# Optimization experiments

Measured on AMD Instinct MI355X. Metric: run time of the kernel, lower is better.

## Reference

```python
import jax, jax.numpy as jnp
import numpy as np

N_NODES = 50000
N_EDGES = 800000
IN_DIM = 256
OUT_DIM = 32
HEADS = 4
NEG_SLOPE = 0.2  # PyG GATConv default
LN_EPS = 1e-5


def setup_inputs() -> dict:
    key = jax.random.key(0)
    ks = jax.random.split(key, 8)
    x = jax.random.normal(ks[0], (N_NODES, IN_DIM), dtype=jnp.float32)
    edge_index = jax.random.randint(ks[1], (2, N_EDGES), 0, N_NODES, dtype=jnp.int64)
    # Glorot-ish scaling for stability
    W = jax.random.normal(ks[2], (IN_DIM, HEADS * OUT_DIM), dtype=jnp.float32) / np.sqrt(IN_DIM)
    att_src = jax.random.normal(ks[3], (HEADS, OUT_DIM), dtype=jnp.float32) / np.sqrt(OUT_DIM)
    att_dst = jax.random.normal(ks[4], (HEADS, OUT_DIM), dtype=jnp.float32) / np.sqrt(OUT_DIM)
    bias = jax.random.normal(ks[5], (HEADS * OUT_DIM,), dtype=jnp.float32) * 0.02
    gamma = jnp.ones((HEADS * OUT_DIM,), dtype=jnp.float32)
    beta = jnp.zeros((HEADS * OUT_DIM,), dtype=jnp.float32)
    return {"x": x, "edge_index": edge_index, "W": W, "att_src": att_src,
            "att_dst": att_dst, "bias": bias, "gamma": gamma, "beta": beta}


def reference(x, edge_index, W, att_src, att_dst, bias, gamma, beta):
    N = x.shape[0]
    H, C = att_src.shape
    # --- GATConv (PyG semantics, eval mode so attention dropout is identity) ---
    # add self-loops (PyG default add_self_loops=True)
    loops = jnp.arange(N, dtype=edge_index.dtype)
    src = jnp.concatenate([edge_index[0], loops])  # [E+N]
    dst = jnp.concatenate([edge_index[1], loops])
    h = (x @ W).reshape(N, H, C)                    # [N,H,C] (lin has no bias)
    a_s = jnp.einsum('nhc,hc->nh', h, att_src)      # [N,H]
    a_d = jnp.einsum('nhc,hc->nh', h, att_dst)
    e = jax.nn.leaky_relu(a_s[src] + a_d[dst], NEG_SLOPE)  # [E+N,H]
    # segment softmax over incoming edges of each destination node
    emax = jax.ops.segment_max(e, dst, num_segments=N)     # every node has a self-loop
    ee = jnp.exp(e - emax[dst])
    denom = jax.ops.segment_sum(ee, dst, num_segments=N)
    alpha = ee / denom[dst]                                 # [E+N,H]
    msg = h[src] * alpha[:, :, None]                        # [E+N,H,C]
    out = jax.ops.segment_sum(msg, dst, num_segments=N).reshape(N, H * C) + bias
    # --- LayerNorm ---
    mu = out.mean(-1, keepdims=True)
    var = ((out - mu) ** 2).mean(-1, keepdims=True)
    out = (out - mu) * jax.lax.rsqrt(var + LN_EPS) * gamma + beta
    # --- dropout (eval: identity) + ELU ---
    return jax.nn.elu(out)
```

## Files before the change

### kernel.cpp

```cpp
#include <hip/hip_runtime.h>
#include <hip/hip_bf16.h>
#include <cstdint>
#include <cstddef>

#define N_NODES 50000
#define N_EDGES 800000
#define IN_DIM 256
#define HC 128
#define HEADS 4
#define NEG_SLOPE 0.2f
#define LN_EPS 1e-5f

#define NGB ((N_NODES + 63) / 64)
#define CAP 64
#define NBUCK 196
#define CAP_PB 32

typedef _Float16 f16x8 __attribute__((ext_vector_type(8)));
typedef _Float16 f16x2 __attribute__((ext_vector_type(2)));
typedef float f32x4 __attribute__((ext_vector_type(4)));

__device__ __forceinline__ float lrelu(float x) { return x > 0.f ? x : NEG_SLOPE * x; }
__device__ __forceinline__ unsigned pack_h2(float a, float b) {
    f16x2 h; h[0] = (_Float16)a; h[1] = (_Float16)b;
    return *(unsigned*)&h;
}

__global__ __launch_bounds__(256) void k_prep_passA(
    const float* __restrict__ W, const int* __restrict__ ei,
    _Float16* __restrict__ W16,
    int* __restrict__ cnt_tab, int2* __restrict__ arena)
{
    __shared__ int cnt[256];
    const int tid = threadIdx.x;
    const int b = blockIdx.x;

    if (b < 16) {
        int c = b * 256 + tid;
        int col = c & 15, quad = (c >> 4) & 3, nt = (c >> 6) & 7, kt = c >> 9;
        int n = nt * 16 + col;
        f16x8 v;
#pragma unroll
        for (int j = 0; j < 8; ++j) {
            int k = kt * 32 + quad * 8 + j;
            v[j] = (_Float16)W[k * HC + n];
        }
        *(f16x8*)(W16 + (size_t)c * 8) = v;
        return;
    }

    const int blk = b - 16;
    const int eb = blk << 10;
    cnt[tid] = 0;
    __syncthreads();
    int src[4], dst[4], rk[4], bk[4];
    bool valid[4];
#pragma unroll
    for (int it = 0; it < 4; ++it) {
        int e = eb + it * 256 + tid;
        valid[it] = (e < N_EDGES);
        src[it] = 0; dst[it] = 0; bk[it] = 0; rk[it] = 0;
        if (valid[it]) {
            src[it] = ei[e];
            dst[it] = ei[N_EDGES + e];
            bk[it]  = dst[it] >> 8;
            rk[it]  = atomicAdd(&cnt[bk[it]], 1);
        }
    }
#pragma unroll
    for (int it = 0; it < 4; ++it) {
        if (valid[it]) {
            int p = ((bk[it] * NGB + blk) << 5) + rk[it];
            arena[p] = (int2){src[it], dst[it]};
        }
    }
    __syncthreads();
    if (tid < NBUCK) cnt_tab[blk * NBUCK + tid] = cnt[tid];
}

__global__ __launch_bounds__(256) void k_gemm(
    const float* __restrict__ x, const _Float16* __restrict__ W16,
    const float* __restrict__ att_src, const float* __restrict__ att_dst,
    _Float16* __restrict__ h16, float* __restrict__ a_s, float* __restrict__ a_d)
{
    __shared__ _Float16 Wlds[32768];
    const int tid = threadIdx.x;

    const int wave = tid >> 6;
    const int lane = tid & 63;
    const int col  = lane & 15;
    const int quad = lane >> 4;
    const int m0   = blockIdx.x * 64 + wave * 16;

    const int rowA = min(m0 + col, N_NODES - 1);
    const float* xrow = x + (size_t)rowA * IN_DIM + quad * 8;

    float4 xr[16];
#pragma unroll
    for (int kt = 0; kt < 8; ++kt) {
        xr[2 * kt]     = *(const float4*)(xrow + kt * 32);
        xr[2 * kt + 1] = *(const float4*)(xrow + kt * 32 + 4);
    }

    {
        const uint4* g4 = (const uint4*)W16;
        uint4* s4 = (uint4*)Wlds;
#pragma unroll
        for (int it = 0; it < 16; ++it) s4[it * 256 + tid] = g4[it * 256 + tid];
    }
    __syncthreads();

    f32x4 acc[8];
#pragma unroll
    for (int nt = 0; nt < 8; ++nt) acc[nt] = (f32x4){0.f, 0.f, 0.f, 0.f};

#pragma unroll
    for (int kt = 0; kt < 8; ++kt) {
        float4 xa = xr[2 * kt], xb = xr[2 * kt + 1];
        f16x8 a;
        a[0] = (_Float16)xa.x; a[1] = (_Float16)xa.y;
        a[2] = (_Float16)xa.z; a[3] = (_Float16)xa.w;
        a[4] = (_Float16)xb.x; a[5] = (_Float16)xb.y;
        a[6] = (_Float16)xb.z; a[7] = (_Float16)xb.w;
#pragma unroll
        for (int nt = 0; nt < 8; ++nt) {
            f16x8 bb = *(const f16x8*)&Wlds[((kt * 8 + nt) * 64 + quad * 16 + col) * 8];
            acc[nt] = __builtin_amdgcn_mfma_f32_16x16x32_f16(a, bb, acc[nt], 0, 0, 0);
        }
    }

    f16x2* h2g = (f16x2*)h16;
#pragma unroll
    for (int a2 = 0; a2 < 4; ++a2) {
#pragma unroll
        for (int r = 0; r < 4; ++r) {
            int row = m0 + quad * 4 + r;
            if (row < N_NODES) {
                f16x2 hv;
                hv[0] = (_Float16)acc[2 * a2][r];
                hv[1] = (_Float16)acc[2 * a2 + 1][r];
                h2g[(size_t)row * 64 + a2 * 16 + col] = hv;
            }
        }
    }

    float pS[4][4], pD[4][4];
#pragma unroll
    for (int hd = 0; hd < 4; ++hd)
#pragma unroll
        for (int r = 0; r < 4; ++r) { pS[hd][r] = 0.f; pD[hd][r] = 0.f; }

#pragma unroll
    for (int nt = 0; nt < 8; ++nt) {
        int ch = nt * 16 + col;
        float sv = att_src[ch], dv = att_dst[ch];
        int hd = nt >> 1;
#pragma unroll
        for (int r = 0; r < 4; ++r) {
            pS[hd][r] += acc[nt][r] * sv;
            pD[hd][r] += acc[nt][r] * dv;
        }
    }
#pragma unroll
    for (int off = 1; off < 16; off <<= 1) {
#pragma unroll
        for (int hd = 0; hd < 4; ++hd)
#pragma unroll
            for (int r = 0; r < 4; ++r) {
                pS[hd][r] += __shfl_xor(pS[hd][r], off, 16);
                pD[hd][r] += __shfl_xor(pD[hd][r], off, 16);
            }
    }
    if (col == 0) {
#pragma unroll
        for (int r = 0; r < 4; ++r) {
            int row = m0 + quad * 4 + r;
            if (row < N_NODES) {
#pragma unroll
                for (int hd = 0; hd < 4; ++hd) {
                    a_s[row * HEADS + hd] = pS[hd][r];
                    a_d[row * HEADS + hd] = pD[hd][r];
                }
            }
        }
    }
}

__global__ __launch_bounds__(1024) void k_bucket(
    const int2* __restrict__ arena, const int* __restrict__ cnt_tab,
    int* __restrict__ rec, int* __restrict__ counts)
{
    __shared__ int cnt[256];
    const int b = blockIdx.x, tid = threadIdx.x;
    if (tid < 256) cnt[tid] = 0;
    __syncthreads();
    if (tid < NGB) {
        int m = cnt_tab[tid * NBUCK + b];
        const int2* seg = arena + (((size_t)b * NGB + tid) << 5);
        for (int i = 0; i < m; ++i) {
            int2 ed = seg[i];
            int r = atomicAdd(&cnt[ed.y & 255], 1);
            rec[((size_t)ed.y << 6) + r] = ed.x;
        }
    }
    __syncthreads();
    if (tid < 256) {
        int n = (b << 8) + tid;
        if (n < N_NODES) counts[n] = cnt[tid];
    }
}

__global__ __launch_bounds__(256) void k_gather(
    const int* __restrict__ counts, const int* __restrict__ rec,
    const float* __restrict__ a_s, const float* __restrict__ a_d,
    const _Float16* __restrict__ h16, const float* __restrict__ bias,
    const float* __restrict__ gamma, const float* __restrict__ beta,
    float* __restrict__ out)
{
    __shared__ int   lsrc[256];
    __shared__ uint2 lw[256];

    int gid = blockIdx.x * 256 + threadIdx.x;
    int n = gid >> 6, lane = gid & 63;
    if (n >= N_NODES) return;

    const int wbase = (threadIdx.x >> 6) * 64;
    const int beg = n << 6;
    const int deg = counts[n];
    const int hd = lane >> 4;
    const f16x2* h2 = (const f16x2*)h16;
    const unsigned short* lwh = (const unsigned short*)&lw[wbase];

    const float4 ad4 = *(const float4*)(a_d + (size_t)n * HEADS);
    const float adh = (hd == 0) ? ad4.x : (hd == 1) ? ad4.y : (hd == 2) ? ad4.z : ad4.w;
    const float wSelf = __expf(lrelu(a_s[n * HEADS + hd] + adh));
    float den = wSelf;
    f16x2 hv = h2[(size_t)n * 64 + lane];
    float acc0 = (float)hv[0] * wSelf;
    float acc1 = (float)hv[1] * wSelf;

    for (int base = 0; base < deg; base += 64) {
        int nc = min(64, deg - base);
        if (lane < nc) {
            int src = rec[beg + base + lane];
            lsrc[wbase + lane] = src;
            float4 s4 = *(const float4*)(a_s + (size_t)src * HEADS);
            float w0 = __expf(lrelu(s4.x + ad4.x));
            float w1 = __expf(lrelu(s4.y + ad4.y));
            float w2 = __expf(lrelu(s4.z + ad4.z));
            float w3 = __expf(lrelu(s4.w + ad4.w));
            lw[wbase + lane] = (uint2){pack_h2(w0, w1), pack_h2(w2, w3)};
        }
        int j = 0;
        for (; j + 8 <= nc; j += 8) {
            int s[8]; float w[8]; f16x2 hh[8];
#pragma unroll
            for (int k = 0; k < 8; ++k) {
                s[k] = lsrc[wbase + j + k];
                unsigned short uw = lwh[(j + k) * 4 + hd];
                _Float16 wf = *(_Float16*)&uw;
                w[k] = (float)wf;
            }
#pragma unroll
            for (int k = 0; k < 8; ++k) hh[k] = h2[(size_t)s[k] * 64 + lane];
#pragma unroll
            for (int k = 0; k < 8; ++k) {
                acc0 += (float)hh[k][0] * w[k];
                acc1 += (float)hh[k][1] * w[k];
                den  += w[k];
            }
        }
        for (; j < nc; ++j) {
            int s0 = lsrc[wbase + j];
            unsigned short uw = lwh[j * 4 + hd];
            _Float16 wf = *(_Float16*)&uw;
            float w0 = (float)wf;
            f16x2 hx = h2[(size_t)s0 * 64 + lane];
            acc0 += (float)hx[0] * w0;
            acc1 += (float)hx[1] * w0;
            den  += w0;
        }
    }

    const int c0 = (lane >> 4) * 32 + (lane & 15);
    const int c1 = c0 + 16;
    float v0 = acc0 / den + bias[c0];
    float v1 = acc1 / den + bias[c1];
    float s = v0 + v1;
#pragma unroll
    for (int off = 32; off; off >>= 1) s += __shfl_xor(s, off, 64);
    float mu = s * (1.f / 128.f);
    float d0 = v0 - mu, d1 = v1 - mu;
    float q = d0 * d0 + d1 * d1;
#pragma unroll
    for (int off = 32; off; off >>= 1) q += __shfl_xor(q, off, 64);
    float rs = rsqrtf(q * (1.f / 128.f) + LN_EPS);
    float o0 = d0 * rs * gamma[c0] + beta[c0];
    float o1 = d1 * rs * gamma[c1] + beta[c1];
    o0 = o0 > 0.f ? o0 : __expf(o0) - 1.f;
    o1 = o1 > 0.f ? o1 : __expf(o1) - 1.f;
    out[(size_t)n * HC + c0] = o0;
    out[(size_t)n * HC + c1] = o1;
}

extern "C" void kernel_launch(void* const* d_in, const int* in_sizes, int n_in,
                              void* d_out, int out_size, void* d_ws, size_t ws_size,
                              hipStream_t stream) {
    const float* x       = (const float*)d_in[0];
    const int*   ei      = (const int*)d_in[1];
    const float* W       = (const float*)d_in[2];
    const float* att_src = (const float*)d_in[3];
    const float* att_dst = (const float*)d_in[4];
    const float* bias    = (const float*)d_in[5];
    const float* gamma   = (const float*)d_in[6];
    const float* beta    = (const float*)d_in[7];
    float* out = (float*)d_out;

    char* ws = (char*)d_ws;
    _Float16* h16     = (_Float16*)(ws);
    float*    a_s     = (float*)(ws + 12800000);
    float*    a_d     = (float*)(ws + 13600000);
    int*      rec     = (int*)  (ws + 14400000);
    int*      counts  = (int*)  (ws + 27200000);
    int*      cnt_tab = (int*)  (ws + 27400000);
    int2*     arena   = (int2*) (ws + 28020000);
    _Float16* W16     = (_Float16*)(ws + 67260000);

    k_prep_passA<<<16 + NGB, 256, 0, stream>>>(W, ei, W16, cnt_tab, arena);
    k_gemm<<<NGB, 256, 0, stream>>>(x, W16, att_src, att_dst, h16, a_s, a_d);
    k_bucket<<<NBUCK, 1024, 0, stream>>>(arena, cnt_tab, rec, counts);
    k_gather<<<(N_NODES * 64 + 255) / 256, 256, 0, stream>>>(
        counts, rec, a_s, a_d, h16, bias, gamma, beta, out);
}
```

Baseline: 177.2 us.

## Fuse GEMM and bucket scatter into one interleaved kernel launch

Merges the projection GEMM and the edge bucketing pass into one kernel. Odd blocks do bucketing and even blocks do a 256-row GEMM tile with 1024 threads. This removes a launch and lets the memory-bound scatter overlap the compute-bound GEMM on the same device. In exchange, GEMM blocks get larger (256 rows each), which cuts GEMM parallelism to about 196 blocks, and each block needs heavier LDS and register use.

```diff
diff --git a/kernel.cpp b/kernel.cpp
--- a/kernel.cpp
+++ b/kernel.cpp
@@ -11,7 +11,8 @@
 #define NEG_SLOPE 0.2f
 #define LN_EPS 1e-5f
 
-#define NGB ((N_NODES + 63) / 64)
+#define NGB ((N_NODES + 255) / 256)
+#define NPB 782
 #define CAP 64
 #define NBUCK 196
 #define CAP_PB 32
@@ -70,7 +71,7 @@
 #pragma unroll
     for (int it = 0; it < 4; ++it) {
         if (valid[it]) {
-            int p = ((bk[it] * NGB + blk) << 5) + rk[it];
+            int p = ((bk[it] * NPB + blk) << 5) + rk[it];
             arena[p] = (int2){src[it], dst[it]};
         }
     }
@@ -78,19 +79,45 @@
     if (tid < NBUCK) cnt_tab[blk * NBUCK + tid] = cnt[tid];
 }
 
-__global__ __launch_bounds__(256) void k_gemm(
+__global__ __launch_bounds__(1024) void k_gemm_bucket(
     const float* __restrict__ x, const _Float16* __restrict__ W16,
     const float* __restrict__ att_src, const float* __restrict__ att_dst,
-    _Float16* __restrict__ h16, float* __restrict__ a_s, float* __restrict__ a_d)
+    _Float16* __restrict__ h16, float* __restrict__ a_s, float* __restrict__ a_d,
+    const int2* __restrict__ arena, const int* __restrict__ cnt_tab,
+    int* __restrict__ rec, int* __restrict__ counts)
 {
     __shared__ _Float16 Wlds[32768];
     const int tid = threadIdx.x;
-
+    const int b = blockIdx.x;
+
+    if (b & 1) {
+        int* cnt = (int*)Wlds;
+        const int bk = b >> 1;
+        if (tid < 256) cnt[tid] = 0;
+        __syncthreads();
+        if (tid < NPB) {
+            int m = cnt_tab[tid * NBUCK + bk];
+            const int2* seg = arena + (((size_t)bk * NPB + tid) << 5);
+            for (int i = 0; i < m; ++i) {
+                int2 ed = seg[i];
+                int r = atomicAdd(&cnt[ed.y & 255], 1);
+                rec[((size_t)ed.y << 6) + r] = ed.x;
+            }
+        }
+        __syncthreads();
+        if (tid < 256) {
+            int n = (bk << 8) + tid;
+            if (n < N_NODES) counts[n] = cnt[tid];
+        }
+        return;
+    }
+
+    const int gb   = b >> 1;
     const int wave = tid >> 6;
     const int lane = tid & 63;
     const int col  = lane & 15;
     const int quad = lane >> 4;
-    const int m0   = blockIdx.x * 64 + wave * 16;
+    const int m0   = gb * 256 + wave * 16;
 
     const int rowA = min(m0 + col, N_NODES - 1);
     const float* xrow = x + (size_t)rowA * IN_DIM + quad * 8;
@@ -106,7 +133,7 @@
         const uint4* g4 = (const uint4*)W16;
         uint4* s4 = (uint4*)Wlds;
 #pragma unroll
-        for (int it = 0; it < 16; ++it) s4[it * 256 + tid] = g4[it * 256 + tid];
+        for (int it = 0; it < 4; ++it) s4[it * 1024 + tid] = g4[it * 1024 + tid];
     }
     __syncthreads();
 
@@ -183,30 +210,6 @@
                 }
             }
         }
-    }
-}
-
-__global__ __launch_bounds__(1024) void k_bucket(
-    const int2* __restrict__ arena, const int* __restrict__ cnt_tab,
-    int* __restrict__ rec, int* __restrict__ counts)
-{
-    __shared__ int cnt[256];
-    const int b = blockIdx.x, tid = threadIdx.x;
-    if (tid < 256) cnt[tid] = 0;
-    __syncthreads();
-    if (tid < NGB) {
-        int m = cnt_tab[tid * NBUCK + b];
-        const int2* seg = arena + (((size_t)b * NGB + tid) << 5);
-        for (int i = 0; i < m; ++i) {
-            int2 ed = seg[i];
-            int r = atomicAdd(&cnt[ed.y & 255], 1);
-            rec[((size_t)ed.y << 6) + r] = ed.x;
-        }
-    }
-    __syncthreads();
-    if (tid < 256) {
-        int n = (b << 8) + tid;
-        if (n < N_NODES) counts[n] = cnt[tid];
     }
 }
 
@@ -326,9 +329,9 @@
     int2*     arena   = (int2*) (ws + 28020000);
     _Float16* W16     = (_Float16*)(ws + 67260000);
 
-    k_prep_passA<<<16 + NGB, 256, 0, stream>>>(W, ei, W16, cnt_tab, arena);
-    k_gemm<<<NGB, 256, 0, stream>>>(x, W16, att_src, att_dst, h16, a_s, a_d);
-    k_bucket<<<NBUCK, 1024, 0, stream>>>(arena, cnt_tab, rec, counts);
+    k_prep_passA<<<16 + NPB, 256, 0, stream>>>(W, ei, W16, cnt_tab, arena);
+    k_gemm_bucket<<<2 * NGB, 1024, 0, stream>>>(
+        x, W16, att_src, att_dst, h16, a_s, a_d, arena, cnt_tab, rec, counts);
     k_gather<<<(N_NODES * 64 + 255) / 256, 256, 0, stream>>>(
         counts, rec, a_s, a_d, h16, bias, gamma, beta, out);
 }
```

New measurement: 179.9 us. Within noise of the previous version (+1.5%).
